# Kernel optimization log

Measured on AMD Instinct MI355X. Metric: run time of the kernel, lower is better.

The kernel has to match this reference:

```python
import jax, jax.numpy as jnp
import numpy as np

DIM = 1024
HEADS = 16
HEAD_DIM = DIM // HEADS          # 64
ROT_DIM = max(16, HEAD_DIM // 2) # 32 (already even)
B, S = 1, 2048


def _linear_params(key, scale=0.02):
    w = jax.random.normal(key, (DIM, DIM), dtype=jnp.float32) * scale
    b = jnp.zeros((DIM,), dtype=jnp.float32)
    return w, b


def setup_inputs() -> dict:
    key = jax.random.key(0)
    ks = jax.random.split(key, 16)
    real = jax.random.normal(ks[0], (B, S, DIM), dtype=jnp.float32)
    imag = jax.random.normal(ks[1], (B, S, DIM), dtype=jnp.float32)
    Wq_r, bq_r = _linear_params(ks[2])
    Wk_r, bk_r = _linear_params(ks[3])
    Wv_r, bv_r = _linear_params(ks[4])
    Wq_i, bq_i = _linear_params(ks[5])
    Wk_i, bk_i = _linear_params(ks[6])
    Wv_i, bv_i = _linear_params(ks[7])
    Wo_r, bo_r = _linear_params(ks[8])
    Wo_i, bo_i = _linear_params(ks[9])
    phase_shifts = jax.random.normal(ks[10], (HEADS, HEAD_DIM), dtype=jnp.float32) * 0.02
    # entanglement init: 0.8*I + 0.1 on super/sub diagonal + 0.1 corners
    ent = np.eye(HEADS, dtype=np.float32) * 0.8
    ent += np.diag(np.ones(HEADS - 1, dtype=np.float32) * 0.1, k=1)
    ent += np.diag(np.ones(HEADS - 1, dtype=np.float32) * 0.1, k=-1)
    ent[0, -1] = 0.1
    ent[-1, 0] = 0.1
    entanglement_matrix = jnp.asarray(ent)
    exponent = np.arange(0, ROT_DIM, 2, dtype=np.float64) / ROT_DIM
    rotary_freqs = jnp.asarray((10000.0 ** (-exponent)).astype(np.float32))
    return {
        'real': real, 'imag': imag,
        'Wq_r': Wq_r, 'bq_r': bq_r, 'Wk_r': Wk_r, 'bk_r': bk_r,
        'Wv_r': Wv_r, 'bv_r': bv_r, 'Wq_i': Wq_i, 'bq_i': bq_i,
        'Wk_i': Wk_i, 'bk_i': bk_i, 'Wv_i': Wv_i, 'bv_i': bv_i,
        'Wo_r': Wo_r, 'bo_r': bo_r, 'Wo_i': Wo_i, 'bo_i': bo_i,
        'phase_shifts': phase_shifts,
        'entanglement_matrix': entanglement_matrix,
        'rotary_freqs': rotary_freqs,
        'interference_strength': jnp.float32(0.0),
        'attention_temperature': jnp.float32(0.0),
        'circle_epsilon': jnp.float32(-2.0),
    }


def _proj(x, W, b):
    # nn.Linear: x @ W^T + b, then split heads -> [B,H,S,Dh]
    y = x @ W.T + b
    return y.reshape(B, S, HEADS, HEAD_DIM).transpose(0, 2, 1, 3)


def _rope(x, cos, sin):
    # x: [B,H,S,Dh]; interleaved pairs rotated over first ROT_DIM dims
    xr, xp = x[..., :ROT_DIM], x[..., ROT_DIM:]
    x1, x2 = xr[..., 0::2], xr[..., 1::2]          # [B,H,S,ROT_DIM//2]
    o1 = x1 * cos - x2 * sin
    o2 = x1 * sin + x2 * cos
    out = jnp.stack([o1, o2], axis=-1).reshape(x.shape[:-1] + (ROT_DIM,))
    return jnp.concatenate([out, xp], axis=-1)


def reference(real, imag, Wq_r, bq_r, Wk_r, bk_r, Wv_r, bv_r,
              Wq_i, bq_i, Wk_i, bk_i, Wv_i, bv_i,
              Wo_r, bo_r, Wo_i, bo_i,
              phase_shifts, entanglement_matrix, rotary_freqs,
              interference_strength, attention_temperature, circle_epsilon):
    q_r = _proj(real, Wq_r, bq_r)
    k_r = _proj(real, Wk_r, bk_r)
    v_r = _proj(real, Wv_r, bv_r)
    q_i = _proj(imag, Wq_i, bq_i)
    k_i = _proj(imag, Wk_i, bk_i)
    v_i = _proj(imag, Wv_i, bv_i)

    # rotary embeddings
    pos = jnp.arange(S, dtype=jnp.float32)
    angles = jnp.outer(pos, rotary_freqs)              # [S, ROT_DIM//2]
    cos = jnp.cos(angles)[None, None]                  # [1,1,S,ROT_DIM//2]
    sin = jnp.sin(angles)[None, None]
    q_r = _rope(q_r, cos, sin); k_r = _rope(k_r, cos, sin)
    q_i = _rope(q_i, cos, sin); k_i = _rope(k_i, cos, sin)

    # entanglement mixing across heads
    q_r = jnp.einsum('bhsd,hx->bxsd', q_r, entanglement_matrix)
    q_i = jnp.einsum('bhsd,hx->bxsd', q_i, entanglement_matrix)
    k_r = jnp.einsum('bhsd,hx->bxsd', k_r, entanglement_matrix)
    k_i = jnp.einsum('bhsd,hx->bxsd', k_i, entanglement_matrix)

    # per-head learned phase shift
    pc = jnp.cos(phase_shifts)[None, :, None, :]       # [1,H,1,Dh]
    ps = jnp.sin(phase_shifts)[None, :, None, :]
    q_r, q_i = q_r * pc - q_i * ps, q_r * ps + q_i * pc
    k_r, k_i = k_r * pc - k_i * ps, k_r * ps + k_i * pc

    # complex attention scores (Karatsuba, as in HAKMEMComplexOperations)
    scale = 1.0 / np.sqrt(HEAD_DIM)
    k1 = jnp.einsum('bhsd,bhtd->bhst', q_r, k_r)
    k2 = jnp.einsum('bhsd,bhtd->bhst', q_i, k_i)
    k3 = jnp.einsum('bhsd,bhtd->bhst', q_r + q_i, k_r + k_i)
    attn_r = (k1 - k2) * scale
    attn_i = (k3 - k1 - k2) * scale

    eps = jax.nn.sigmoid(circle_epsilon) * 0.03
    ar = attn_r + eps * attn_i
    ai = attn_i - eps * attn_r
    attn_mag = jnp.sqrt(ar * ar + ai * ai + 1e-6)

    causal = jnp.triu(jnp.ones((S, S), dtype=bool), k=1)[None, None]
    attn_mag = jnp.where(causal, -jnp.inf, attn_mag)

    temp = jnp.clip(jnp.exp(attention_temperature), 0.1, None)
    strength = jax.nn.sigmoid(interference_strength)
    attn = jax.nn.softmax(attn_mag * strength / temp, axis=-1)
    attn = jnp.nan_to_num(attn)

    # complex_matmul(attn, 0, v_r, v_i) -> (attn@v_r, attn@v_i)
    out_r = jnp.einsum('bhst,bhtd->bhsd', attn, v_r)
    out_i = jnp.einsum('bhst,bhtd->bhsd', attn, v_i)
    out_r = out_r.transpose(0, 2, 1, 3).reshape(B, S, DIM)
    out_i = out_i.transpose(0, 2, 1, 3).reshape(B, S, DIM)
    out_r = out_r @ Wo_r.T + bo_r
    out_i = out_i @ Wo_i.T + bo_i
    return out_r, out_i
```

## Files before the change

### kernel.cpp

```cpp
#include <hip/hip_runtime.h>
#include <cstddef>
#include <cstdint>
#include <math.h>

#define S_LEN 2048
#define DIM 1024
#define NH 16
#define HD 64

typedef __attribute__((ext_vector_type(8))) short bf16x8;
typedef __attribute__((ext_vector_type(8))) unsigned short u16x8;
typedef __attribute__((ext_vector_type(4))) float f32x4;

__device__ inline unsigned short f2bf(float x) {
  union { float f; unsigned u; } v; v.f = x;
  unsigned r = v.u + 0x7FFFu + ((v.u >> 16) & 1u);
  return (unsigned short)(r >> 16);
}
__device__ inline float bf2f(unsigned short x) {
  union { unsigned u; float f; } v; v.u = ((unsigned)x) << 16; return v.f;
}

#define GLOAD_LDS16(g, l)                                              \
  __builtin_amdgcn_global_load_lds(                                    \
      (const __attribute__((address_space(1))) void*)(g),              \
      (__attribute__((address_space(3))) void*)(l), 16, 0, 0)

struct ConvBatch {
  const float* src[10];
  unsigned short* dst[10];
  int n[10];
  int fold[10];
};

__global__ __launch_bounds__(256) void conv_kernel(ConvBatch cb,
                                                   const float* __restrict__ E)
{
  __shared__ float Es[NH * NH];
  const int t = threadIdx.x;
  Es[t] = E[t];
  __syncthreads();

  const int y = blockIdx.y;
  const int flat = (blockIdx.x * 256 + t) * 8;
  if (flat >= cb.n[y]) return;
  const float* s = cb.src[y];

  if (!cb.fold[y]) {
    float4 a = *(const float4*)(s + flat);
    float4 b = *(const float4*)(s + flat + 4);
    u16x8 o;
    o[0] = f2bf(a.x); o[1] = f2bf(a.y); o[2] = f2bf(a.z); o[3] = f2bf(a.w);
    o[4] = f2bf(b.x); o[5] = f2bf(b.y); o[6] = f2bf(b.z); o[7] = f2bf(b.w);
    *(u16x8*)(cb.dst[y] + flat) = o;
  } else {
    const int row = flat >> 10;
    const int k0  = flat & 1023;
    const int x = row >> 6, d = row & 63;
    float acc[8] = {};
#pragma unroll
    for (int h = 0; h < NH; h++) {
      const float e = Es[h * NH + x];
      const float* p = s + ((size_t)((h << 6) + d) << 10) + k0;
      float4 a = *(const float4*)p;
      float4 b = *(const float4*)(p + 4);
      acc[0] += e * a.x; acc[1] += e * a.y; acc[2] += e * a.z; acc[3] += e * a.w;
      acc[4] += e * b.x; acc[5] += e * b.y; acc[6] += e * b.z; acc[7] += e * b.w;
    }
    u16x8 o;
#pragma unroll
    for (int j = 0; j < 8; j++) o[j] = f2bf(acc[j]);
    *(u16x8*)(cb.dst[y] + flat) = o;
  }
}

__global__ __launch_bounds__(256) void bias_fold_kernel(
    const float* __restrict__ b0, const float* __restrict__ b1,
    const float* __restrict__ b2, const float* __restrict__ b3,
    const float* __restrict__ E, float* __restrict__ out)
{
  __shared__ float Es[NH * NH];
  const int t = threadIdx.x;
  Es[t] = E[t];
  __syncthreads();
  const float* srcs[4] = {b0, b1, b2, b3};
  for (int idx = t; idx < 4096; idx += 256) {
    const int tz = idx >> 10, nn = idx & 1023;
    const int x = nn >> 6, d = nn & 63;
    const float* b = srcs[tz];
    float acc = 0.f;
#pragma unroll
    for (int h = 0; h < NH; h++) acc += Es[h * NH + x] * b[h * 64 + d];
    out[idx] = acc;
  }
}

__global__ __launch_bounds__(256) void prep_tabs_kernel(
    const float* __restrict__ freqs, const float* __restrict__ phase,
    float2* __restrict__ ropeTab, float2* __restrict__ phaseTab)
{
  const int idx = blockIdx.x * 256 + threadIdx.x;
  if (idx < 32768) {
    const int s = idx >> 4, j = idx & 15;
    float sn, cs;
    sincosf((float)s * freqs[j], &sn, &cs);
    ropeTab[idx] = make_float2(cs, sn);
  } else if (idx < 32768 + 1024) {
    const int k = idx - 32768;
    float sn, cs;
    sincosf(phase[k], &sn, &cs);
    phaseTab[k] = make_float2(cs, sn);
  }
}

struct BGemm {
  const unsigned short* A[6];
  const unsigned short* W[6];
  const float* bias[6];
  void* C[6];
  int mode[6];
};

__global__ __launch_bounds__(256) void gemm_mfma_kernel(BGemm gb)
{
  constexpr int K = DIM;
  const int z = blockIdx.z;
  const unsigned short* __restrict__ A = gb.A[z];
  const unsigned short* __restrict__ W = gb.W[z];
  const float* __restrict__ bias = gb.bias[z];
  const int mode = gb.mode[z];

  __shared__ __align__(16) unsigned short As[128 * 32];
  __shared__ __align__(16) unsigned short Ws[128 * 32];

  const int t    = threadIdx.x;
  const int lane = t & 63;
  const int w    = t >> 6;
  const int wm   = w >> 1, wn = w & 1;
  const int quad = lane >> 4, lcol = lane & 15;
  const int m0   = blockIdx.y * 128;
  const int n0   = blockIdx.x * 128;

  const int srow = t >> 2;
  const int sk8  = (t & 3) * 8;

  f32x4 acc[4][4];
#pragma unroll
  for (int i = 0; i < 4; i++)
#pragma unroll
    for (int j = 0; j < 4; j++)
#pragma unroll
      for (int r = 0; r < 4; r++) acc[i][j][r] = 0.f;

  for (int k0 = 0; k0 < K; k0 += 32) {
    __syncthreads();
#pragma unroll
    for (int p = 0; p < 2; p++) {
      const unsigned short* ga = A + (size_t)(m0 + p * 64 + srow) * K + k0 + sk8;
      GLOAD_LDS16(ga, As + (size_t)(p * 256 + w * 64) * 8);
      const unsigned short* gw = W + (size_t)(n0 + p * 64 + srow) * K + k0 + sk8;
      GLOAD_LDS16(gw, Ws + (size_t)(p * 256 + w * 64) * 8);
    }
    __syncthreads();

    bf16x8 af[4], bfr[4];
#pragma unroll
    for (int mi = 0; mi < 4; mi++)
      af[mi] = *(const bf16x8*)&As[(wm * 64 + mi * 16 + lcol) * 32 + quad * 8];
#pragma unroll
    for (int ni = 0; ni < 4; ni++)
      bfr[ni] = *(const bf16x8*)&Ws[(wn * 64 + ni * 16 + lcol) * 32 + quad * 8];
#pragma unroll
    for (int mi = 0; mi < 4; mi++)
#pragma unroll
      for (int ni = 0; ni < 4; ni++)
        acc[mi][ni] = __builtin_amdgcn_mfma_f32_16x16x32_bf16(af[mi], bfr[ni], acc[mi][ni], 0, 0, 0);
  }

#pragma unroll
  for (int mi = 0; mi < 4; mi++) {
#pragma unroll
    for (int ni = 0; ni < 4; ni++) {
#pragma unroll
      for (int r = 0; r < 4; r++) {
        const int grow = m0 + wm * 64 + mi * 16 + quad * 4 + r;
        const int gcol = n0 + wn * 64 + ni * 16 + lcol;
        const float v = acc[mi][ni][r] + bias[gcol];
        if (mode == 0) {
          ((float*)gb.C[z])[(size_t)grow * DIM + gcol] = v;
        } else if (mode == 1) {
          const int hh = gcol >> 6, d = gcol & 63;
          ((unsigned short*)gb.C[z])[((size_t)hh * S_LEN + grow) * HD + d] = f2bf(v);
        } else {
          const int hh = gcol >> 6, d = gcol & 63;
          ((unsigned short*)gb.C[z])[((size_t)hh * HD + d) * S_LEN + grow] = f2bf(v);
        }
      }
    }
  }
}

__global__ __launch_bounds__(256) void ropephase_kernel(
    unsigned short* q_r, unsigned short* q_i,
    unsigned short* k_r, unsigned short* k_i,
    const float2* __restrict__ ropeTab, const float2* __restrict__ phaseTab)
{
  const int z = blockIdx.y;
  unsigned short* R = z ? k_r : q_r;
  unsigned short* I = z ? k_i : q_i;

  const int flat = blockIdx.x * 256 + threadIdx.x;
  const int x   = flat >> 14;
  const int rem = flat & 16383;
  const int s   = rem >> 3;
  const int d0  = (rem & 7) * 8;

  const size_t base = ((size_t)x * S_LEN + s) * HD + d0;
  bf16x8 r8 = *(const bf16x8*)(R + base);
  bf16x8 i8 = *(const bf16x8*)(I + base);
  float a[8], b[8];
#pragma unroll
  for (int e = 0; e < 8; e++) {
    a[e] = bf2f((unsigned short)r8[e]);
    b[e] = bf2f((unsigned short)i8[e]);
  }

  if (d0 < 32) {
#pragma unroll
    for (int jj = 0; jj < 8; jj += 2) {
      const int j = (d0 + jj) >> 1;
      const float2 cs = ropeTab[s * 16 + j];
      const float a1 = a[jj], a2 = a[jj + 1];
      const float b1 = b[jj], b2 = b[jj + 1];
      a[jj]     = a1 * cs.x - a2 * cs.y;
      a[jj + 1] = a1 * cs.y + a2 * cs.x;
      b[jj]     = b1 * cs.x - b2 * cs.y;
      b[jj + 1] = b1 * cs.y + b2 * cs.x;
    }
  }

  u16x8 orr, oii;
#pragma unroll
  for (int e = 0; e < 8; e++) {
    const float2 pp = phaseTab[x * HD + d0 + e];
    orr[e] = f2bf(a[e] * pp.x - b[e] * pp.y);
    oii[e] = f2bf(a[e] * pp.y + b[e] * pp.x);
  }
  *(u16x8*)(R + base) = orr;
  *(u16x8*)(I + base) = oii;
}

#define LDK 72

__global__ __launch_bounds__(256) void flash_mfma_kernel(
    const unsigned short* __restrict__ Qr, const unsigned short* __restrict__ Qi,
    const unsigned short* __restrict__ Kr, const unsigned short* __restrict__ Ki,
    const unsigned short* __restrict__ VtR, const unsigned short* __restrict__ VtI,
    float* __restrict__ OpR, float* __restrict__ OpI, float* __restrict__ Lp,
    const float* __restrict__ p_is, const float* __restrict__ p_at,
    const float* __restrict__ p_ce)
{
  __shared__ __align__(16) unsigned short Krs[64 * LDK];
  __shared__ __align__(16) unsigned short Kis[64 * LDK];
  __shared__ __align__(16) unsigned short VTr[64 * LDK];
  __shared__ __align__(16) unsigned short VTi[64 * LDK];
  __shared__ __align__(16) unsigned short Ps [64 * LDK];

  const int t    = threadIdx.x;
  const int lane = t & 63;
  const int w    = t >> 6;
  const int quad = lane >> 4;
  const int lcol = lane & 15;

  const int bx    = blockIdx.x;
  const int p     = bx >> 1;
  const int half  = bx & 1;
  const int itile = 31 - (p >> 4);
  const int h     = p & 15;
  const int i0    = itile * 64;
  const int n     = itile + 1;
  const int jmid  = (n + 1) >> 1;
  const int jbeg  = half ? jmid : 0;
  const int jend  = half ? n : jmid;

  const float strength = 1.f / (1.f + expf(-p_is[0]));
  const float temp     = fmaxf(expf(p_at[0]), 0.1f);
  const float cfac     = strength / temp;
  const float eps      = 0.03f / (1.f + expf(-p_ce[0]));
  const float c2       = 0.015625f * (1.f + eps * eps);

  const int srow = t >> 3;
  const int sd0  = (t & 7) * 8;

  bf16x8 qrf[2], qif[2];
  {
    const int qrow = i0 + w * 16 + lcol;
    const size_t base_q = ((size_t)h * S_LEN + qrow) * HD;
#pragma unroll
    for (int ks = 0; ks < 2; ks++) {
      qrf[ks] = *(const bf16x8*)(Qr + base_q + ks * 32 + quad * 8);
      qif[ks] = *(const bf16x8*)(Qi + base_q + ks * 32 + quad * 8);
    }
  }

  float lsum[4] = {0.f, 0.f, 0.f, 0.f};
  f32x4 aOr[4], aOi[4];
#pragma unroll
  for (int cc = 0; cc < 4; cc++)
#pragma unroll
    for (int r = 0; r < 4; r++) { aOr[cc][r] = 0.f; aOi[cc][r] = 0.f; }

  bf16x8 pk[2], pki[2], pv[2], pvi[2];

  if (jbeg < jend) {
    const int j0 = jbeg * 64;
    const size_t kb = ((size_t)h * S_LEN + j0) * HD;
#pragma unroll
    for (int it = 0; it < 2; it++) {
      const int row = srow + it * 32;
      pk [it] = *(const bf16x8*)(Kr  + kb + (size_t)row * HD + sd0);
      pki[it] = *(const bf16x8*)(Ki  + kb + (size_t)row * HD + sd0);
      pv [it] = *(const bf16x8*)(VtR + ((size_t)h * HD + row) * S_LEN + j0 + sd0);
      pvi[it] = *(const bf16x8*)(VtI + ((size_t)h * HD + row) * S_LEN + j0 + sd0);
    }
  }

  for (int jt = jbeg; jt < jend; jt++) {
    __syncthreads();
#pragma unroll
    for (int it = 0; it < 2; it++) {
      const int row = srow + it * 32;
      *(bf16x8*)&Krs[row * LDK + sd0] = pk [it];
      *(bf16x8*)&Kis[row * LDK + sd0] = pki[it];
      *(bf16x8*)&VTr[row * LDK + sd0] = pv [it];
      *(bf16x8*)&VTi[row * LDK + sd0] = pvi[it];
    }
    __syncthreads();

    if (jt + 1 < jend) {
      const int j0n = (jt + 1) * 64;
      const size_t kb = ((size_t)h * S_LEN + j0n) * HD;
#pragma unroll
      for (int it = 0; it < 2; it++) {
        const int row = srow + it * 32;
        pk [it] = *(const bf16x8*)(Kr  + kb + (size_t)row * HD + sd0);
        pki[it] = *(const bf16x8*)(Ki  + kb + (size_t)row * HD + sd0);
        pv [it] = *(const bf16x8*)(VtR + ((size_t)h * HD + row) * S_LEN + j0n + sd0);
        pvi[it] = *(const bf16x8*)(VtI + ((size_t)h * HD + row) * S_LEN + j0n + sd0);
      }
    }

    f32x4 k1[4], k2[4], kx[4];
#pragma unroll
    for (int cc = 0; cc < 4; cc++)
#pragma unroll
      for (int r = 0; r < 4; r++) { k1[cc][r] = 0.f; k2[cc][r] = 0.f; kx[cc][r] = 0.f; }
#pragma unroll
    for (int ks = 0; ks < 2; ks++) {
#pragma unroll
      for (int cc = 0; cc < 4; cc++) {
        const int off = (cc * 16 + lcol) * LDK + ks * 32 + quad * 8;
        bf16x8 krf = *(const bf16x8*)&Krs[off];
        bf16x8 kif = *(const bf16x8*)&Kis[off];
        k1[cc] = __builtin_amdgcn_mfma_f32_16x16x32_bf16(qrf[ks], krf, k1[cc], 0, 0, 0);
        k2[cc] = __builtin_amdgcn_mfma_f32_16x16x32_bf16(qif[ks], kif, k2[cc], 0, 0, 0);
        kx[cc] = __builtin_amdgcn_mfma_f32_16x16x32_bf16(qrf[ks], kif, kx[cc], 0, 0, 0);
        kx[cc] = __builtin_amdgcn_mfma_f32_16x16x32_bf16(qif[ks], krf, kx[cc], 0, 0, 0);
      }
    }

    const bool diag = (jt == itile);
    const int j0 = jt * 64;
#pragma unroll
    for (int r = 0; r < 4; r++) {
      const int prow = (w * 16 + quad * 4 + r) * LDK;
      float rs = 0.f;
#pragma unroll
      for (int cc = 0; cc < 4; cc++) {
        const float a = k1[cc][r] - k2[cc][r];
        const float b = kx[cc][r];
        const float u = fmaf(b, b, a * a);
        const float mag = sqrtf(fmaf(u, c2, 1e-6f));
        float pp = __expf(mag * cfac);
        if (diag) {
          const int gi = i0 + w * 16 + quad * 4 + r;
          const int gj = j0 + cc * 16 + lcol;
          if (gj > gi) pp = 0.f;
        }
        Ps[prow + cc * 16 + lcol] = f2bf(pp);
        rs += pp;
      }
      lsum[r] += rs;
    }

#pragma unroll
    for (int ks = 0; ks < 2; ks++) {
      bf16x8 pf = *(const bf16x8*)&Ps[(w * 16 + lcol) * LDK + ks * 32 + quad * 8];
#pragma unroll
      for (int cc = 0; cc < 4; cc++) {
        const int off = (cc * 16 + lcol) * LDK + ks * 32 + quad * 8;
        bf16x8 vrf = *(const bf16x8*)&VTr[off];
        bf16x8 vif = *(const bf16x8*)&VTi[off];
        aOr[cc] = __builtin_amdgcn_mfma_f32_16x16x32_bf16(pf, vrf, aOr[cc], 0, 0, 0);
        aOi[cc] = __builtin_amdgcn_mfma_f32_16x16x32_bf16(pf, vif, aOi[cc], 0, 0, 0);
      }
    }
  }

  const size_t SLsz = (size_t)S_LEN * DIM;
#pragma unroll
  for (int r = 0; r < 4; r++) {
    float rs = lsum[r];
#pragma unroll
    for (int off = 1; off < 16; off <<= 1)
      rs += __shfl_xor(rs, off, 16);
    const int row = i0 + w * 16 + quad * 4 + r;
    if (lcol == 0)
      Lp[((size_t)half * NH + h) * S_LEN + row] = rs;
  }
#pragma unroll
  for (int cc = 0; cc < 4; cc++) {
#pragma unroll
    for (int r = 0; r < 4; r++) {
      const int row = i0 + w * 16 + quad * 4 + r;
      const int col = h * HD + cc * 16 + lcol;
      OpR[half * SLsz + (size_t)row * DIM + col] = aOr[cc][r];
      OpI[half * SLsz + (size_t)row * DIM + col] = aOi[cc][r];
    }
  }
}

__global__ __launch_bounds__(256) void combine_kernel(
    const float* __restrict__ OpR, const float* __restrict__ OpI,
    const float* __restrict__ Lp,
    unsigned short* __restrict__ Or, unsigned short* __restrict__ Oi)
{
  const size_t SLsz = (size_t)S_LEN * DIM;
  const int idx = blockIdx.x * 256 + threadIdx.x;
  const size_t e0 = (size_t)idx * 4;
  const int s = (int)(e0 >> 10);
  const int col = (int)(e0 & 1023);
  const int h = col >> 6;

  const float L = Lp[(size_t)h * S_LEN + s] + Lp[((size_t)NH + h) * S_LEN + s];
  const float inv = 1.f / L;

  float4 r0 = *(const float4*)(OpR + e0);
  float4 r1 = *(const float4*)(OpR + SLsz + e0);
  float4 i0 = *(const float4*)(OpI + e0);
  float4 i1 = *(const float4*)(OpI + SLsz + e0);

  ushort4 orv, oiv;
  orv.x = f2bf((r0.x + r1.x) * inv); orv.y = f2bf((r0.y + r1.y) * inv);
  orv.z = f2bf((r0.z + r1.z) * inv); orv.w = f2bf((r0.w + r1.w) * inv);
  oiv.x = f2bf((i0.x + i1.x) * inv); oiv.y = f2bf((i0.y + i1.y) * inv);
  oiv.z = f2bf((i0.z + i1.z) * inv); oiv.w = f2bf((i0.w + i1.w) * inv);
  *(ushort4*)(Or + e0) = orv;
  *(ushort4*)(Oi + e0) = oiv;
}

extern "C" void kernel_launch(void* const* d_in, const int* in_sizes, int n_in,
                              void* d_out, int out_size, void* d_ws, size_t ws_size,
                              hipStream_t stream)
{
  const float* real = (const float*)d_in[0];
  const float* imag = (const float*)d_in[1];
  const float* Wq_r = (const float*)d_in[2];
  const float* bq_r = (const float*)d_in[3];
  const float* Wk_r = (const float*)d_in[4];
  const float* bk_r = (const float*)d_in[5];
  const float* Wv_r = (const float*)d_in[6];
  const float* bv_r = (const float*)d_in[7];
  const float* Wq_i = (const float*)d_in[8];
  const float* bq_i = (const float*)d_in[9];
  const float* Wk_i = (const float*)d_in[10];
  const float* bk_i = (const float*)d_in[11];
  const float* Wv_i = (const float*)d_in[12];
  const float* bv_i = (const float*)d_in[13];
  const float* Wo_r = (const float*)d_in[14];
  const float* bo_r = (const float*)d_in[15];
  const float* Wo_i = (const float*)d_in[16];
  const float* bo_i = (const float*)d_in[17];
  const float* phase = (const float*)d_in[18];
  const float* ent   = (const float*)d_in[19];
  const float* freqs = (const float*)d_in[20];
  const float* p_is  = (const float*)d_in[21];
  const float* p_at  = (const float*)d_in[22];
  const float* p_ce  = (const float*)d_in[23];

  unsigned short* ws = (unsigned short*)d_ws;
  const size_t SL = (size_t)S_LEN * DIM;
  const size_t WL = (size_t)DIM * DIM;

  unsigned short* realb = ws;
  unsigned short* imagb = realb + SL;
  unsigned short* Wb    = imagb + SL;
  unsigned short* q_r   = Wb + 8 * WL;
  unsigned short* k_r   = q_r + SL;
  unsigned short* v_r   = k_r + SL;
  unsigned short* q_i   = v_r + SL;
  unsigned short* k_i   = q_i + SL;
  unsigned short* v_i   = k_i + SL;

  float* fbase   = (float*)(v_i + SL);
  float* biasf   = fbase;
  float* ropeTab = biasf + 4096;
  float* phaseTb = ropeTab + 65536;
  float* OpR     = phaseTb + 2048;
  float* OpI     = OpR + 2 * SL;
  float* Lp      = OpI + 2 * SL;

  unsigned short* O_r = q_r;
  unsigned short* O_i = q_i;

  float* out_r = (float*)d_out;
  float* out_i = out_r + SL;

  ConvBatch cb;
  cb.src[0] = real; cb.dst[0] = realb; cb.n[0] = (int)SL; cb.fold[0] = 0;
  cb.src[1] = imag; cb.dst[1] = imagb; cb.n[1] = (int)SL; cb.fold[1] = 0;
  const float* wsrc[8] = {Wq_r, Wk_r, Wv_r, Wq_i, Wk_i, Wv_i, Wo_r, Wo_i};
  const int wfold[8]   = {1,    1,    0,    1,    1,    0,    0,    0};
  for (int i = 0; i < 8; i++) {
    cb.src[2 + i] = wsrc[i];
    cb.dst[2 + i] = Wb + (size_t)i * WL;
    cb.n[2 + i] = (int)WL;
    cb.fold[2 + i] = wfold[i];
  }
  conv_kernel<<<dim3(1024, 10), dim3(256), 0, stream>>>(cb, ent);

  bias_fold_kernel<<<dim3(1), dim3(256), 0, stream>>>(bq_r, bk_r, bq_i, bk_i, ent, biasf);

  prep_tabs_kernel<<<dim3(132), dim3(256), 0, stream>>>(
      freqs, phase, (float2*)ropeTab, (float2*)phaseTb);

  BGemm g1;
  g1.A[0] = realb; g1.A[1] = realb; g1.A[2] = realb;
  g1.A[3] = imagb; g1.A[4] = imagb; g1.A[5] = imagb;
  for (int i = 0; i < 6; i++) g1.W[i] = Wb + (size_t)i * WL;
  g1.bias[0] = biasf;        g1.bias[1] = biasf + 1024; g1.bias[2] = bv_r;
  g1.bias[3] = biasf + 2048; g1.bias[4] = biasf + 3072; g1.bias[5] = bv_i;
  g1.C[0] = q_r; g1.C[1] = k_r; g1.C[2] = v_r;
  g1.C[3] = q_i; g1.C[4] = k_i; g1.C[5] = v_i;
  g1.mode[0] = 1; g1.mode[1] = 1; g1.mode[2] = 2;
  g1.mode[3] = 1; g1.mode[4] = 1; g1.mode[5] = 2;
  gemm_mfma_kernel<<<dim3(8, 16, 6), dim3(256), 0, stream>>>(g1);

  ropephase_kernel<<<dim3(1024, 2), dim3(256), 0, stream>>>(
      q_r, q_i, k_r, k_i, (const float2*)ropeTab, (const float2*)phaseTb);

  flash_mfma_kernel<<<dim3(1024), dim3(256), 0, stream>>>(
      q_r, q_i, k_r, k_i, v_r, v_i, OpR, OpI, Lp, p_is, p_at, p_ce);

  combine_kernel<<<dim3(2048), dim3(256), 0, stream>>>(OpR, OpI, Lp, O_r, O_i);

  BGemm g2 = {};
  g2.A[0] = O_r; g2.A[1] = O_i;
  g2.W[0] = Wb + 6 * WL; g2.W[1] = Wb + 7 * WL;
  g2.bias[0] = bo_r; g2.bias[1] = bo_i;
  g2.C[0] = out_r; g2.C[1] = out_i;
  g2.mode[0] = 0; g2.mode[1] = 0;
  gemm_mfma_kernel<<<dim3(8, 16, 2), dim3(256), 0, stream>>>(g2);
}
```

Baseline: 308.3 us.

## Fuse RoPE into QKV GEMM epilogue, fold phase into Q, use bf16 partials

```diff
diff --git a/kernel.cpp b/kernel.cpp
--- a/kernel.cpp
+++ b/kernel.cpp
@@ -33,8 +33,13 @@
   int fold[10];
 };
 
-__global__ __launch_bounds__(256) void conv_kernel(ConvBatch cb,
-                                                   const float* __restrict__ E)
+__global__ __launch_bounds__(256) void conv_kernel(
+    ConvBatch cb, const float* __restrict__ E,
+    const float* __restrict__ freqs, const float* __restrict__ phase,
+    const float* __restrict__ bq_r, const float* __restrict__ bk_r,
+    const float* __restrict__ bq_i, const float* __restrict__ bk_i,
+    float* __restrict__ biasf, float2* __restrict__ ropeTab,
+    float2* __restrict__ phaseTab2)
 {
   __shared__ float Es[NH * NH];
   const int t = threadIdx.x;
@@ -42,6 +47,32 @@
   __syncthreads();
 
   const int y = blockIdx.y;
+
+  if (y == 10) {
+    const int idx = blockIdx.x * 256 + t;
+    if (idx < 32768) {
+      const int s = idx >> 4, j = idx & 15;
+      float sn, cs;
+      sincosf((float)s * freqs[j], &sn, &cs);
+      ropeTab[idx] = make_float2(cs, sn);
+    } else if (idx < 32768 + 1024) {
+      const int k = idx - 32768;
+      float sn, cs;
+      sincosf(2.f * phase[k], &sn, &cs);
+      phaseTab2[k] = make_float2(cs, sn);
+    } else if (idx < 32768 + 1024 + 4096) {
+      const int i = idx - 33792;
+      const int tz = i >> 10, nn = i & 1023;
+      const int x = nn >> 6, d = nn & 63;
+      const float* b = (tz == 0) ? bq_r : (tz == 1) ? bk_r : (tz == 2) ? bq_i : bk_i;
+      float acc = 0.f;
+#pragma unroll
+      for (int h = 0; h < NH; h++) acc += Es[h * NH + x] * b[h * 64 + d];
+      biasf[i] = acc;
+    }
+    return;
+  }
+
   const int flat = (blockIdx.x * 256 + t) * 8;
   if (flat >= cb.n[y]) return;
   const float* s = cb.src[y];
@@ -74,51 +105,13 @@
   }
 }
 
-__global__ __launch_bounds__(256) void bias_fold_kernel(
-    const float* __restrict__ b0, const float* __restrict__ b1,
-    const float* __restrict__ b2, const float* __restrict__ b3,
-    const float* __restrict__ E, float* __restrict__ out)
-{
-  __shared__ float Es[NH * NH];
-  const int t = threadIdx.x;
-  Es[t] = E[t];
-  __syncthreads();
-  const float* srcs[4] = {b0, b1, b2, b3};
-  for (int idx = t; idx < 4096; idx += 256) {
-    const int tz = idx >> 10, nn = idx & 1023;
-    const int x = nn >> 6, d = nn & 63;
-    const float* b = srcs[tz];
-    float acc = 0.f;
-#pragma unroll
-    for (int h = 0; h < NH; h++) acc += Es[h * NH + x] * b[h * 64 + d];
-    out[idx] = acc;
-  }
-}
-
-__global__ __launch_bounds__(256) void prep_tabs_kernel(
-    const float* __restrict__ freqs, const float* __restrict__ phase,
-    float2* __restrict__ ropeTab, float2* __restrict__ phaseTab)
-{
-  const int idx = blockIdx.x * 256 + threadIdx.x;
-  if (idx < 32768) {
-    const int s = idx >> 4, j = idx & 15;
-    float sn, cs;
-    sincosf((float)s * freqs[j], &sn, &cs);
-    ropeTab[idx] = make_float2(cs, sn);
-  } else if (idx < 32768 + 1024) {
-    const int k = idx - 32768;
-    float sn, cs;
-    sincosf(phase[k], &sn, &cs);
-    phaseTab[k] = make_float2(cs, sn);
-  }
-}
-
 struct BGemm {
   const unsigned short* A[6];
   const unsigned short* W[6];
   const float* bias[6];
   void* C[6];
   int mode[6];
+  const float2* ropeTab;
 };
 
 __global__ __launch_bounds__(256) void gemm_mfma_kernel(BGemm gb)
@@ -185,69 +178,28 @@
       for (int r = 0; r < 4; r++) {
         const int grow = m0 + wm * 64 + mi * 16 + quad * 4 + r;
         const int gcol = n0 + wn * 64 + ni * 16 + lcol;
-        const float v = acc[mi][ni][r] + bias[gcol];
+        float v = acc[mi][ni][r] + bias[gcol];
+        if (mode == 3) {
+          const float vp = __shfl_xor(v, 1);
+          const int d = gcol & 63;
+          if (d < 32) {
+            const float2 cs = gb.ropeTab[grow * 16 + (d >> 1)];
+            v = (d & 1) ? (v * cs.x + vp * cs.y)
+                        : (v * cs.x - vp * cs.y);
+          }
+        }
         if (mode == 0) {
           ((float*)gb.C[z])[(size_t)grow * DIM + gcol] = v;
-        } else if (mode == 1) {
+        } else if (mode == 2) {
+          const int hh = gcol >> 6, d = gcol & 63;
+          ((unsigned short*)gb.C[z])[((size_t)hh * HD + d) * S_LEN + grow] = f2bf(v);
+        } else {
           const int hh = gcol >> 6, d = gcol & 63;
           ((unsigned short*)gb.C[z])[((size_t)hh * S_LEN + grow) * HD + d] = f2bf(v);
-        } else {
-          const int hh = gcol >> 6, d = gcol & 63;
-          ((unsigned short*)gb.C[z])[((size_t)hh * HD + d) * S_LEN + grow] = f2bf(v);
         }
       }
     }
   }
-}
-
-__global__ __launch_bounds__(256) void ropephase_kernel(
-    unsigned short* q_r, unsigned short* q_i,
-    unsigned short* k_r, unsigned short* k_i,
-    const float2* __restrict__ ropeTab, const float2* __restrict__ phaseTab)
-{
-  const int z = blockIdx.y;
-  unsigned short* R = z ? k_r : q_r;
-  unsigned short* I = z ? k_i : q_i;
-
-  const int flat = blockIdx.x * 256 + threadIdx.x;
-  const int x   = flat >> 14;
-  const int rem = flat & 16383;
-  const int s   = rem >> 3;
-  const int d0  = (rem & 7) * 8;
-
-  const size_t base = ((size_t)x * S_LEN + s) * HD + d0;
-  bf16x8 r8 = *(const bf16x8*)(R + base);
-  bf16x8 i8 = *(const bf16x8*)(I + base);
-  float a[8], b[8];
-#pragma unroll
-  for (int e = 0; e < 8; e++) {
-    a[e] = bf2f((unsigned short)r8[e]);
-    b[e] = bf2f((unsigned short)i8[e]);
-  }
-
-  if (d0 < 32) {
-#pragma unroll
-    for (int jj = 0; jj < 8; jj += 2) {
-      const int j = (d0 + jj) >> 1;
-      const float2 cs = ropeTab[s * 16 + j];
-      const float a1 = a[jj], a2 = a[jj + 1];
-      const float b1 = b[jj], b2 = b[jj + 1];
-      a[jj]     = a1 * cs.x - a2 * cs.y;
-      a[jj + 1] = a1 * cs.y + a2 * cs.x;
-      b[jj]     = b1 * cs.x - b2 * cs.y;
-      b[jj + 1] = b1 * cs.y + b2 * cs.x;
-    }
-  }
-
-  u16x8 orr, oii;
-#pragma unroll
-  for (int e = 0; e < 8; e++) {
-    const float2 pp = phaseTab[x * HD + d0 + e];
-    orr[e] = f2bf(a[e] * pp.x - b[e] * pp.y);
-    oii[e] = f2bf(a[e] * pp.y + b[e] * pp.x);
-  }
-  *(u16x8*)(R + base) = orr;
-  *(u16x8*)(I + base) = oii;
 }
 
 #define LDK 72
@@ -256,7 +208,8 @@
     const unsigned short* __restrict__ Qr, const unsigned short* __restrict__ Qi,
     const unsigned short* __restrict__ Kr, const unsigned short* __restrict__ Ki,
     const unsigned short* __restrict__ VtR, const unsigned short* __restrict__ VtI,
-    float* __restrict__ OpR, float* __restrict__ OpI, float* __restrict__ Lp,
+    unsigned short* __restrict__ OpR, unsigned short* __restrict__ OpI,
+    float* __restrict__ Lp, const float2* __restrict__ phaseTab2,
     const float* __restrict__ p_is, const float* __restrict__ p_at,
     const float* __restrict__ p_ce)
 {
@@ -264,7 +217,7 @@
   __shared__ __align__(16) unsigned short Kis[64 * LDK];
   __shared__ __align__(16) unsigned short VTr[64 * LDK];
   __shared__ __align__(16) unsigned short VTi[64 * LDK];
-  __shared__ __align__(16) unsigned short Ps [64 * LDK];
+  unsigned short* Ps = Krs;
 
   const int t    = threadIdx.x;
   const int lane = t & 63;
@@ -298,8 +251,19 @@
     const size_t base_q = ((size_t)h * S_LEN + qrow) * HD;
 #pragma unroll
     for (int ks = 0; ks < 2; ks++) {
-      qrf[ks] = *(const bf16x8*)(Qr + base_q + ks * 32 + quad * 8);
-      qif[ks] = *(const bf16x8*)(Qi + base_q + ks * 32 + quad * 8);
+      bf16x8 r8 = *(const bf16x8*)(Qr + base_q + ks * 32 + quad * 8);
+      bf16x8 i8 = *(const bf16x8*)(Qi + base_q + ks * 32 + quad * 8);
+      bf16x8 orr, oii;
+#pragma unroll
+      for (int j = 0; j < 8; j++) {
+        const float2 ph = phaseTab2[h * HD + ks * 32 + quad * 8 + j];
+        const float qr = bf2f((unsigned short)r8[j]);
+        const float qi = bf2f((unsigned short)i8[j]);
+        orr[j] = (short)f2bf(qr * ph.x - qi * ph.y);
+        oii[j] = (short)f2bf(qr * ph.y + qi * ph.x);
+      }
+      qrf[ks] = orr;
+      qif[ks] = oii;
     }
   }
 
@@ -368,6 +332,8 @@
         kx[cc] = __builtin_amdgcn_mfma_f32_16x16x32_bf16(qif[ks], krf, kx[cc], 0, 0, 0);
       }
     }
+
+    __syncthreads();
 
     const bool diag = (jt == itile);
     const int j0 = jt * 64;
@@ -424,20 +390,20 @@
     for (int r = 0; r < 4; r++) {
       const int row = i0 + w * 16 + quad * 4 + r;
       const int col = h * HD + cc * 16 + lcol;
-      OpR[half * SLsz + (size_t)row * DIM + col] = aOr[cc][r];
-      OpI[half * SLsz + (size_t)row * DIM + col] = aOi[cc][r];
+      OpR[half * SLsz + (size_t)row * DIM + col] = f2bf(aOr[cc][r]);
+      OpI[half * SLsz + (size_t)row * DIM + col] = f2bf(aOi[cc][r]);
     }
   }
 }
 
 __global__ __launch_bounds__(256) void combine_kernel(
-    const float* __restrict__ OpR, const float* __restrict__ OpI,
+    const unsigned short* __restrict__ OpR, const unsigned short* __restrict__ OpI,
     const float* __restrict__ Lp,
     unsigned short* __restrict__ Or, unsigned short* __restrict__ Oi)
 {
   const size_t SLsz = (size_t)S_LEN * DIM;
   const int idx = blockIdx.x * 256 + threadIdx.x;
-  const size_t e0 = (size_t)idx * 4;
+  const size_t e0 = (size_t)idx * 8;
   const int s = (int)(e0 >> 10);
   const int col = (int)(e0 & 1023);
   const int h = col >> 6;
@@ -445,18 +411,19 @@
   const float L = Lp[(size_t)h * S_LEN + s] + Lp[((size_t)NH + h) * S_LEN + s];
   const float inv = 1.f / L;
 
-  float4 r0 = *(const float4*)(OpR + e0);
-  float4 r1 = *(const float4*)(OpR + SLsz + e0);
-  float4 i0 = *(const float4*)(OpI + e0);
-  float4 i1 = *(const float4*)(OpI + SLsz + e0);
-
-  ushort4 orv, oiv;
-  orv.x = f2bf((r0.x + r1.x) * inv); orv.y = f2bf((r0.y + r1.y) * inv);
-  orv.z = f2bf((r0.z + r1.z) * inv); orv.w = f2bf((r0.w + r1.w) * inv);
-  oiv.x = f2bf((i0.x + i1.x) * inv); oiv.y = f2bf((i0.y + i1.y) * inv);
-  oiv.z = f2bf((i0.z + i1.z) * inv); oiv.w = f2bf((i0.w + i1.w) * inv);
-  *(ushort4*)(Or + e0) = orv;
-  *(ushort4*)(Oi + e0) = oiv;
+  bf16x8 r0 = *(const bf16x8*)(OpR + e0);
+  bf16x8 r1 = *(const bf16x8*)(OpR + SLsz + e0);
+  bf16x8 i0 = *(const bf16x8*)(OpI + e0);
+  bf16x8 i1 = *(const bf16x8*)(OpI + SLsz + e0);
+
+  u16x8 orv, oiv;
+#pragma unroll
+  for (int j = 0; j < 8; j++) {
+    orv[j] = f2bf((bf2f((unsigned short)r0[j]) + bf2f((unsigned short)r1[j])) * inv);
+    oiv[j] = f2bf((bf2f((unsigned short)i0[j]) + bf2f((unsigned short)i1[j])) * inv);
+  }
+  *(u16x8*)(Or + e0) = orv;
+  *(u16x8*)(Oi + e0) = oiv;
 }
 
 extern "C" void kernel_launch(void* const* d_in, const int* in_sizes, int n_in,
@@ -501,14 +468,14 @@
   unsigned short* q_i   = v_r + SL;
   unsigned short* k_i   = q_i + SL;
   unsigned short* v_i   = k_i + SL;
-
-  float* fbase   = (float*)(v_i + SL);
-  float* biasf   = fbase;
-  float* ropeTab = biasf + 4096;
-  float* phaseTb = ropeTab + 65536;
-  float* OpR     = phaseTb + 2048;
-  float* OpI     = OpR + 2 * SL;
-  float* Lp      = OpI + 2 * SL;
+  unsigned short* OpR   = v_i + SL;
+  unsigned short* OpI   = OpR + 2 * SL;
+
+  float* fbase    = (float*)(OpI + 2 * SL);
+  float* biasf    = fbase;
+  float* ropeTab  = biasf + 4096;
+  float* phaseTb2 = ropeTab + 65536;
+  float* Lp       = phaseTb2 + 2048;
 
   unsigned short* O_r = q_r;
   unsigned short* O_i = q_i;
@@ -527,12 +494,9 @@
     cb.n[2 + i] = (int)WL;
     cb.fold[2 + i] = wfold[i];
   }
-  conv_kernel<<<dim3(1024, 10), dim3(256), 0, stream>>>(cb, ent);
-
-  bias_fold_kernel<<<dim3(1), dim3(256), 0, stream>>>(bq_r, bk_r, bq_i, bk_i, ent, biasf);
-
-  prep_tabs_kernel<<<dim3(132), dim3(256), 0, stream>>>(
-      freqs, phase, (float2*)ropeTab, (float2*)phaseTb);
+  conv_kernel<<<dim3(1024, 11), dim3(256), 0, stream>>>(
+      cb, ent, freqs, phase, bq_r, bk_r, bq_i, bk_i,
+      biasf, (float2*)ropeTab, (float2*)phaseTb2);
 
   BGemm g1;
   g1.A[0] = realb; g1.A[1] = realb; g1.A[2] = realb;
@@ -542,17 +506,16 @@
   g1.bias[3] = biasf + 2048; g1.bias[4] = biasf + 3072; g1.bias[5] = bv_i;
   g1.C[0] = q_r; g1.C[1] = k_r; g1.C[2] = v_r;
   g1.C[3] = q_i; g1.C[4] = k_i; g1.C[5] = v_i;
-  g1.mode[0] = 1; g1.mode[1] = 1; g1.mode[2] = 2;
-  g1.mode[3] = 1; g1.mode[4] = 1; g1.mode[5] = 2;
+  g1.mode[0] = 3; g1.mode[1] = 3; g1.mode[2] = 2;
+  g1.mode[3] = 3; g1.mode[4] = 3; g1.mode[5] = 2;
+  g1.ropeTab = (const float2*)ropeTab;
   gemm_mfma_kernel<<<dim3(8, 16, 6), dim3(256), 0, stream>>>(g1);
 
-  ropephase_kernel<<<dim3(1024, 2), dim3(256), 0, stream>>>(
-      q_r, q_i, k_r, k_i, (const float2*)ropeTab, (const float2*)phaseTb);
-
   flash_mfma_kernel<<<dim3(1024), dim3(256), 0, stream>>>(
-      q_r, q_i, k_r, k_i, v_r, v_i, OpR, OpI, Lp, p_is, p_at, p_ce);
-
-  combine_kernel<<<dim3(2048), dim3(256), 0, stream>>>(OpR, OpI, Lp, O_r, O_i);
+      q_r, q_i, k_r, k_i, v_r, v_i, OpR, OpI, Lp,
+      (const float2*)phaseTb2, p_is, p_at, p_ce);
+
+  combine_kernel<<<dim3(1024), dim3(256), 0, stream>>>(OpR, OpI, Lp, O_r, O_i);
 
   BGemm g2 = {};
   g2.A[0] = O_r; g2.A[1] = O_i;
@@ -560,5 +523,6 @@
   g2.bias[0] = bo_r; g2.bias[1] = bo_i;
   g2.C[0] = out_r; g2.C[1] = out_i;
   g2.mode[0] = 0; g2.mode[1] = 0;
+  g2.ropeTab = (const float2*)ropeTab;
   gemm_mfma_kernel<<<dim3(8, 16, 2), dim3(256), 0, stream>>>(g2);
 }
```

After: 291.2 us. 1.06x faster.
